# Optimization experiments

Measured on AMD Instinct MI355X. Metric: run time of the kernel, lower is better.

Reference implementation:

```python
import jax, jax.numpy as jnp
import numpy as np

# Model dims: nSet=48, nItemMax=80, input feat=512,
# D = baseChn*max_channel_ratio = 128 = head_size, H = num_heads = 2.
S, N, DIN = 48, 80, 512
D = 128
H, HS = 2, 128
EPS = 1e-3  # layer_normalization epsilon (non-set-norm branch)

def _w(key, fi, fo):
    return jax.random.normal(key, (fi, fo), jnp.float32) / np.sqrt(fi)

def setup_inputs() -> dict:
    key = jax.random.key(0)
    ks = jax.random.split(key, 20)
    sizes = jax.random.randint(ks[0], (S,), 1, N + 1)
    x = jax.random.normal(ks[1], (S, N, DIN), jnp.float32)
    item_mask = (jnp.arange(N)[None, :] < sizes[:, None]).astype(jnp.float32)
    x = x * item_mask[:, :, None]  # zero-pad invalid items (drives ==0 masks)
    return {
        "x": x,
        "x_size": sizes.astype(jnp.float32),
        # trainable MLP (fc1/fc2/fc3, gelu, no bias)
        "W1": _w(ks[2], DIN, 512),
        "W2": _w(ks[3], 512, 256),
        "W3": _w(ks[4], 256, D),
        # encoder self-attention layer
        "Wq_s": _w(ks[5], D, H * HS),
        "Wk_s": _w(ks[6], D, H * HS),
        "Wv_s": _w(ks[7], D, H * HS),
        "Wh_s": _w(ks[8], H * HS, HS),
        "Wfc_e": _w(ks[9], D, D),
        # decoder cross-set attention layer
        "Wq_c": _w(ks[10], D, H * HS),
        "Wk_c": _w(ks[11], D, H * HS),
        "Wv_c": _w(ks[12], D, H * HS),
        "Wh_c": _w(ks[13], H * HS, HS),
        "Wfc_d": _w(ks[14], D, D),
        # cross_set_score
        "Wcs": _w(ks[15], D, H * HS),
        "Wcs2": _w(ks[16], H, 1),
    }

def _gelu(z):
    return jax.nn.gelu(z, approximate=False)  # tf.nn.gelu default

def _item_norm(x):
    # layer_normalization with is_set_norm=False: per-item LN, zero padded rows
    mean = jnp.mean(x, axis=-1, keepdims=True)
    std = jnp.std(x, axis=-1, keepdims=True)
    norm = (x - mean) / (std + EPS)
    keep = jnp.sum(x, axis=-1, keepdims=True) != 0
    return jnp.where(keep, norm, jnp.zeros_like(x))

def _masked_softmax(s):
    # faithful to source: mask entries where raw score == 0
    m = s != 0
    e = jnp.where(m, jnp.exp(s - jnp.max(s, axis=-1, keepdims=True)), 0.0)
    return e / (jnp.sum(e, axis=-1, keepdims=True) + 1e-10)

def _mha(q_in, kv_in, Wq, Wk, Wv, Wh):
    # q_in/kv_in: [S, S, N, D]
    q = (q_in @ Wq).reshape(S, S, N, H, HS)
    k = (kv_in @ Wk).reshape(S, S, N, H, HS)
    v = (kv_in @ Wv).reshape(S, S, N, H, HS)
    s = jnp.einsum('xynhd,xymhd->xyhnm', q, k) / np.sqrt(HS)
    a = _masked_softmax(s)
    o = jnp.einsum('xyhnm,xymhd->xynhd', a, v).reshape(S, S, N, H * HS)
    return o @ Wh  # -> [S, S, N, HS]

def reference(x, x_size, W1, W2, W3, Wq_s, Wk_s, Wv_s, Wh_s, Wfc_e,
              Wq_c, Wk_c, Wv_c, Wh_c, Wfc_d, Wcs, Wcs2):
    # item-wise MLP projection: feat -> 512 -> 256 -> 128
    h = _gelu(_gelu(_gelu(x @ W1) @ W2) @ W3)  # [S, N, D]
    # pairwise set grid [nSet_x, nSet_y, nItemMax, D]
    x4 = jnp.broadcast_to(h[:, None], (S, S, N, D))
    # encoder: self-attention over items within each (i,j) pair
    z = _item_norm(x4)
    x4 = x4 + _mha(z, z, Wq_s, Wk_s, Wv_s, Wh_s)
    z = _item_norm(x4)
    x4 = x4 + _gelu(z @ Wfc_e)
    # decoder: cross-set attention, out[i,j] = Attn(q=z[i,j], kv=z[j,i])
    z = _item_norm(x4)
    x4 = x4 + _mha(z, jnp.transpose(z, (1, 0, 2, 3)), Wq_c, Wk_c, Wv_c, Wh_c)
    z = _item_norm(x4)
    x4 = x4 + _gelu(z @ Wfc_d)
    # cross_set_score: pairwise ReLU-matmul, set-size normalized
    xh = (x4 @ Wcs).reshape(S, S, N, H, HS).transpose(0, 1, 3, 2, 4)  # [j,i,h,n,d]
    A = jax.nn.relu(jnp.einsum('jihnd,ijhmd->jihnm', xh, xh) / np.sqrt(HS))
    sc = A.sum((-1, -2)) / x_size[None, :, None] / x_size[:, None, None]  # [S,S,H]
    return sc @ Wcs2  # [S, S, 1]
```

## Files before the change

### kernel.cpp

```cpp
#include <hip/hip_runtime.h>
#include <hip/hip_bf16.h>


#define SS 48
#define NI 80

typedef unsigned short us;
typedef __attribute__((ext_vector_type(8))) short s8v;
typedef __attribute__((ext_vector_type(4))) float f4v;

#define MFMA(a,b,c) __builtin_amdgcn_mfma_f32_16x16x32_bf16((a),(b),(c),0,0,0)

__device__ __forceinline__ float gelu_f(float x){
  return 0.5f * x * (1.0f + erff(x * 0.7071067811865475f));
}
__device__ __forceinline__ us f2b(float f){
  __hip_bfloat16 b = __float2bfloat16(f);
  return reinterpret_cast<us&>(b);
}
__device__ __forceinline__ s8v zero8(){ s8v v = {0,0,0,0,0,0,0,0}; return v; }
__device__ __forceinline__ void gl16(const void* g, void* l){
  __builtin_amdgcn_global_load_lds(
      (const __attribute__((address_space(1))) void*)g,
      (__attribute__((address_space(3))) void*)l, 16, 0, 0);
}

template<int ABF16, int OUTF32>
__global__ __launch_bounds__(256) void mgemm_k(const void* __restrict__ Ap,
    const float* __restrict__ B, void* __restrict__ Cp, int N, int K)
{
  __shared__ __align__(16) char lds[10240];
  char* As = lds; char* Bs = lds + 5120;
  const int t = threadIdx.x;
  const int wv = t >> 6, lm = t & 15, lh = (t >> 4) & 3;
  const int bx = blockIdx.x, by = blockIdx.y;
  const int ar = wv*16 + lm, r0 = wv*16 + lh*4;
  f4v acc[4];
#pragma unroll
  for (int ct = 0; ct < 4; ++ct) acc[ct] = {0.f,0.f,0.f,0.f};
  const int rA = t >> 2, kcA = (t & 3) << 3;
  const int kkB = t >> 3, nnB = (t & 7) << 3;
  for (int k0 = 0; k0 < K; k0 += 32) {
    __syncthreads();
    if (ABF16) {
      s8v v = *(const s8v*)((const us*)Ap + (size_t)(by*64 + rA)*K + k0 + kcA);
      *(s8v*)(As + rA*80 + kcA*2) = v;
    } else {
      const float* ap = (const float*)Ap + (size_t)(by*64 + rA)*K + k0 + kcA;
      float4 v0 = *(const float4*)ap, v1 = *(const float4*)(ap + 4);
      us tmp[8] = {f2b(v0.x),f2b(v0.y),f2b(v0.z),f2b(v0.w),
                   f2b(v1.x),f2b(v1.y),f2b(v1.z),f2b(v1.w)};
      *(s8v*)(As + rA*80 + kcA*2) = *(const s8v*)tmp;
    }
    {
      const float* bp = B + (size_t)(k0 + kkB)*N + bx*64 + nnB;
      float4 w0 = *(const float4*)bp, w1 = *(const float4*)(bp + 4);
      float w8[8] = {w0.x,w0.y,w0.z,w0.w,w1.x,w1.y,w1.z,w1.w};
#pragma unroll
      for (int q = 0; q < 8; ++q)
        *(us*)(Bs + (nnB + q)*80 + kkB*2) = f2b(w8[q]);
    }
    __syncthreads();
    s8v af = *(const s8v*)(As + ar*80 + lh*16);
#pragma unroll
    for (int ct = 0; ct < 4; ++ct) {
      s8v bf = *(const s8v*)(Bs + (ct*16 + lm)*80 + lh*16);
      acc[ct] = MFMA(af, bf, acc[ct]);
    }
  }
#pragma unroll
  for (int ct = 0; ct < 4; ++ct)
#pragma unroll
    for (int reg = 0; reg < 4; ++reg) {
      size_t r = by*64 + r0 + reg;
      int c = bx*64 + ct*16 + lm;
      float v = gelu_f(acc[ct][reg]);
      if (OUTF32) ((float*)Cp)[r*N + c] = v;
      else ((us*)Cp)[r*N + c] = f2b(v);
    }
}

__global__ __launch_bounds__(256) void qkv_k(const us* __restrict__ A,
    const float* __restrict__ Wq, const float* __restrict__ Wk,
    const float* __restrict__ Wv, us* __restrict__ Qb, us* __restrict__ Kb,
    us* __restrict__ VT)
{
  __shared__ __align__(16) char lds[10240];
  char* As = lds; char* Bs = lds + 5120;
  const int t = threadIdx.x;
  const int wv = t >> 6, lm = t & 15, lh = (t >> 4) & 3;
  const int bx = blockIdx.x, by = blockIdx.y;
  const int sel = bx >> 2, bxx = bx & 3;
  const float* B = sel == 0 ? Wq : (sel == 1 ? Wk : Wv);
  const int ar = wv*16 + lm, r0 = wv*16 + lh*4;
  f4v acc[4];
#pragma unroll
  for (int ct = 0; ct < 4; ++ct) acc[ct] = {0.f,0.f,0.f,0.f};
  const int rA = t >> 2, kcA = (t & 3) << 3;
  const int kkB = t >> 3, nnB = (t & 7) << 3;
#pragma unroll
  for (int k0 = 0; k0 < 128; k0 += 32) {
    __syncthreads();
    {
      s8v v = *(const s8v*)(A + (size_t)(by*64 + rA)*128 + k0 + kcA);
      *(s8v*)(As + rA*80 + kcA*2) = v;
      const float* bp = B + (size_t)(k0 + kkB)*256 + bxx*64 + nnB;
      float4 w0 = *(const float4*)bp, w1 = *(const float4*)(bp + 4);
      float w8[8] = {w0.x,w0.y,w0.z,w0.w,w1.x,w1.y,w1.z,w1.w};
#pragma unroll
      for (int q = 0; q < 8; ++q)
        *(us*)(Bs + (nnB + q)*80 + kkB*2) = f2b(w8[q]);
    }
    __syncthreads();
    s8v af = *(const s8v*)(As + ar*80 + lh*16);
#pragma unroll
    for (int ct = 0; ct < 4; ++ct) {
      s8v bf = *(const s8v*)(Bs + (ct*16 + lm)*80 + lh*16);
      acc[ct] = MFMA(af, bf, acc[ct]);
    }
  }
  if (sel < 2) {
    us* O = sel ? Kb : Qb;
#pragma unroll
    for (int ct = 0; ct < 4; ++ct)
#pragma unroll
      for (int reg = 0; reg < 4; ++reg)
        O[(size_t)(by*64 + r0 + reg)*256 + bxx*64 + ct*16 + lm] = f2b(acc[ct][reg]);
  } else {
#pragma unroll
    for (int ct = 0; ct < 4; ++ct)
#pragma unroll
      for (int reg = 0; reg < 4; ++reg) {
        int r = by*64 + r0 + reg;
        int s = r / 80, m = r % 80;
        int d = bxx*64 + ct*16 + lm;
        VT[((size_t)s*256 + d)*80 + m] = f2b(acc[ct][reg]);
      }
  }
}

__global__ __launch_bounds__(64) void norm_k(const float* __restrict__ in,
                                             us* __restrict__ out)
{
  const int r = blockIdx.x, t = threadIdx.x;
  float v0 = in[(size_t)r*128 + t];
  float v1 = in[(size_t)r*128 + t + 64];
  float sm = v0 + v1;
#pragma unroll
  for (int off = 1; off < 64; off <<= 1) sm += __shfl_xor(sm, off, 64);
  float mean = sm * (1.0f/128.0f);
  float d0 = v0 - mean, d1 = v1 - mean;
  float vs = d0*d0 + d1*d1;
#pragma unroll
  for (int off = 1; off < 64; off <<= 1) vs += __shfl_xor(vs, off, 64);
  float inv = 1.0f / (sqrtf(vs * (1.0f/128.0f)) + 1e-3f);
  bool keep = (sm != 0.0f);
  out[(size_t)r*128 + t]      = f2b(keep ? d0*inv : 0.0f);
  out[(size_t)r*128 + t + 64] = f2b(keep ? d1*inv : 0.0f);
}

__global__ __launch_bounds__(128) void prep_k(
    const float* __restrict__ Wh_s, const float* __restrict__ Wfc_e,
    const float* __restrict__ Wh_c, const float* __restrict__ Wfc_d,
    const float* __restrict__ Wcs,  const float* __restrict__ Wv_s,
    const float* __restrict__ Wv_c,
    us* __restrict__ WfcTe, us* __restrict__ WfcTd,
    float* __restrict__ Wvh_s, float* __restrict__ Wvh_c,
    us* __restrict__ Mb)
{
  const int x = blockIdx.x, task = blockIdx.y, tid = threadIdx.x;
  if (task == 0) {
    WfcTe[x*128 + tid] = f2b(Wfc_e[(size_t)tid*128 + x]);
  } else if (task == 1) {
    WfcTd[x*128 + tid] = f2b(Wfc_d[(size_t)tid*128 + x]);
  } else if (task < 6) {
    int h = (task - 2) & 1;
    const float* Wv = task < 4 ? Wv_s : Wv_c;
    const float* Wh = task < 4 ? Wh_s : Wh_c;
    float* Wvh = task < 4 ? Wvh_s : Wvh_c;
    float acc = 0.f;
#pragma unroll 8
    for (int d = 0; d < 128; ++d)
      acc = fmaf(Wv[(size_t)x*256 + h*128 + d], Wh[(size_t)(h*128 + d)*128 + tid], acc);
    Wvh[(size_t)x*256 + h*128 + tid] = acc;
  } else {
    int h = task - 6;
    float acc = 0.f;
#pragma unroll 8
    for (int k = 0; k < 128; ++k)
      acc = fmaf(Wcs[(size_t)x*256 + h*128 + k], Wcs[(size_t)tid*256 + h*128 + k], acc);
    Mb[(size_t)h*16384 + x*128 + tid] = f2b(acc);
  }
}

__device__ __forceinline__ void attn4e(int a, int t,
    const us* __restrict__ Qg, const us* __restrict__ Kg,
    const us* __restrict__ VTg, const float* __restrict__ baseg,
    const us* __restrict__ WfcT,
    char* __restrict__ X, char* __restrict__ Y, f4v x4[8])
{
  const int wv = t >> 6, lane = t & 63, lm = t & 15, lh = (t >> 4) & 3;
  const int ar = wv*16 + lm, r0 = wv*16 + lh*4;
  const float isq = 0.08838834764831845f;
  const int b = a;
#pragma unroll
  for (int dt = 0; dt < 8; ++dt) x4[dt] = (f4v){0.f,0.f,0.f,0.f};

#pragma unroll 1
  for (int h = 0; h < 2; ++h) {
    if (h == 1) __syncthreads();
#pragma unroll
    for (int c = 0; c < 4; ++c) {
      int chunk = wv*4 + c;
      int row = chunk*4 + (lane >> 4);
      int scb = ((lane & 15) << 4) ^ ((row & 7) << 4);
      gl16(Kg + (((size_t)(b*NI + row)) << 8) + h*128 + (scb >> 1), X + chunk*1024);
    }
    s8v qf[4];
    {
      const us* qrow = Qg + (((size_t)(a*NI + ar)) << 8) + h*128 + lh*8;
#pragma unroll
      for (int ks = 0; ks < 4; ++ks) qf[ks] = *(const s8v*)(qrow + ks*32);
    }
    __syncthreads();
    f4v sA[5];
#pragma unroll
    for (int nt = 0; nt < 5; ++nt) {
      int row = nt*16 + lm;
      f4v acc = (f4v){0.f,0.f,0.f,0.f};
#pragma unroll
      for (int ks = 0; ks < 4; ++ks) {
        s8v kf = *(const s8v*)(X + row*256 + ((ks*64 + lh*16) ^ ((row & 7) << 4)));
        acc = MFMA(qf[ks], kf, acc);
      }
      sA[nt] = acc;
    }
#pragma unroll
    for (int reg = 0; reg < 4; ++reg) {
      int r = r0 + reg;
      float sv[5];
#pragma unroll
      for (int nt = 0; nt < 5; ++nt) sv[nt] = sA[nt][reg] * isq;
      float mx = sv[0];
#pragma unroll
      for (int nt = 1; nt < 5; ++nt) mx = fmaxf(mx, sv[nt]);
#pragma unroll
      for (int off = 1; off < 16; off <<= 1) mx = fmaxf(mx, __shfl_xor(mx, off, 64));
      float e[5], sum = 0.f;
#pragma unroll
      for (int nt = 0; nt < 5; ++nt) {
        e[nt] = (sv[nt] != 0.f) ? __expf(sv[nt] - mx) : 0.f;
        sum += e[nt];
      }
#pragma unroll
      for (int off = 1; off < 16; off <<= 1) sum += __shfl_xor(sum, off, 64);
      float inv = 1.f / (sum + 1e-10f);
#pragma unroll
      for (int nt = 0; nt < 5; ++nt)
        *(us*)(Y + r*256 + ((2*(nt*16 + lm)) ^ ((r & 7) << 4))) = f2b(e[nt] * inv);
    }
    s8v pf0 = *(const s8v*)(Y + ar*256 + ((lh*16) ^ ((ar & 7) << 4)));
    s8v pf1 = *(const s8v*)(Y + ar*256 + ((64 + lh*16) ^ ((ar & 7) << 4)));
    s8v pf2 = zero8();
    if (lh < 2)
      pf2 = *(const s8v*)(Y + ar*256 + ((128 + lh*16) ^ ((ar & 7) << 4)));
    __syncthreads();
#pragma unroll
    for (int c = 0; c < 4; ++c) {
      int chunk = wv*4 + c;
      int L = chunk*1024 + lane*16;
      int rv = L / 160;
      int rem = L - rv*160;
      int cv = (rem >> 4) - (rv % 10); if (cv < 0) cv += 10;
      gl16(VTg + ((size_t)(b*256 + h*128 + rv))*80 + (cv << 3), X + chunk*1024);
    }
    __syncthreads();
#pragma unroll
    for (int dt = 0; dt < 8; ++dt) {
      int row = dt*16 + lm;
      int rm = (row % 10) << 4;
      int o0 = lh*16 + rm; if (o0 >= 160) o0 -= 160;
      x4[dt] = MFMA(pf0, *(const s8v*)(X + row*160 + o0), x4[dt]);
      int o1 = 64 + lh*16 + rm; if (o1 >= 160) o1 -= 160;
      x4[dt] = MFMA(pf1, *(const s8v*)(X + row*160 + o1), x4[dt]);
      s8v v2 = zero8();
      if (lh < 2) {
        int o2 = 128 + lh*16 + rm; if (o2 >= 160) o2 -= 160;
        v2 = *(const s8v*)(X + row*160 + o2);
      }
      x4[dt] = MFMA(pf2, v2, x4[dt]);
    }
    if (h == 1) {
#pragma unroll
      for (int reg = 0; reg < 4; ++reg) {
        int r = r0 + reg;
#pragma unroll
        for (int dt = 0; dt < 8; ++dt)
          x4[dt][reg] += baseg[(((size_t)(a*NI + r)) << 7) + dt*16 + lm];
      }
    }
  }

  __syncthreads();
  for (int chunk = wv; chunk < 16; chunk += 5) {
    int row = chunk*4 + (lane >> 4);
    int scb = ((lane & 15) << 4) ^ ((row & 7) << 4);
    gl16(WfcT + (size_t)row*128 + (scb >> 1), X + chunk*1024);
  }
#pragma unroll
  for (int reg = 0; reg < 4; ++reg) {
    int r = r0 + reg;
    float sm = 0.f;
#pragma unroll
    for (int dt = 0; dt < 8; ++dt) sm += x4[dt][reg];
#pragma unroll
    for (int off = 1; off < 16; off <<= 1) sm += __shfl_xor(sm, off, 64);
    float mean = sm * (1.0f/128.0f);
    float vs = 0.f;
#pragma unroll
    for (int dt = 0; dt < 8; ++dt) { float d = x4[dt][reg] - mean; vs = fmaf(d, d, vs); }
#pragma unroll
    for (int off = 1; off < 16; off <<= 1) vs += __shfl_xor(vs, off, 64);
    float inv = 1.f / (sqrtf(vs * (1.0f/128.0f)) + 1e-3f);
    bool keep = (sm != 0.f);
#pragma unroll
    for (int dt = 0; dt < 8; ++dt)
      *(us*)(Y + r*256 + ((2*(dt*16 + lm)) ^ ((r & 7) << 4))) = f2b(keep ? (x4[dt][reg]-mean)*inv : 0.f);
  }
  s8v zf[4];
#pragma unroll
  for (int ks = 0; ks < 4; ++ks)
    zf[ks] = *(const s8v*)(Y + ar*256 + ((ks*64 + lh*16) ^ ((ar & 7) << 4)));
  __syncthreads();
#pragma unroll
  for (int dt = 0; dt < 4; ++dt) {
    int row = dt*16 + lm;
    f4v acc = (f4v){0.f,0.f,0.f,0.f};
#pragma unroll
    for (int ks = 0; ks < 4; ++ks) {
      s8v wfr = *(const s8v*)(X + row*256 + ((ks*64 + lh*16) ^ ((row & 7) << 4)));
      acc = MFMA(zf[ks], wfr, acc);
    }
#pragma unroll
    for (int reg = 0; reg < 4; ++reg) x4[dt][reg] += gelu_f(acc[reg]);
  }
  __syncthreads();
  for (int chunk = wv; chunk < 16; chunk += 5) {
    int row = chunk*4 + (lane >> 4);
    int scb = ((lane & 15) << 4) ^ ((row & 7) << 4);
    gl16(WfcT + (size_t)(row + 64)*128 + (scb >> 1), X + chunk*1024);
  }
  __syncthreads();
#pragma unroll
  for (int dt = 4; dt < 8; ++dt) {
    int row = dt*16 + lm;
    int r2 = row - 64;
    f4v acc = (f4v){0.f,0.f,0.f,0.f};
#pragma unroll
    for (int ks = 0; ks < 4; ++ks) {
      s8v wfr = *(const s8v*)(X + r2*256 + ((ks*64 + lh*16) ^ ((row & 7) << 4)));
      acc = MFMA(zf[ks], wfr, acc);
    }
#pragma unroll
    for (int reg = 0; reg < 4; ++reg) x4[dt][reg] += gelu_f(acc[reg]);
  }
}

__global__ __launch_bounds__(320) void enc_k(
    const us* __restrict__ Qg, const us* __restrict__ Kg,
    const us* __restrict__ VTg, const float* __restrict__ hb,
    const us* __restrict__ WfcT, float* __restrict__ e2p,
    us* __restrict__ z3b)
{
  __shared__ __align__(16) char X[20480];
  __shared__ __align__(16) char Y[20480];
  const int t = threadIdx.x;
  const int wv = t >> 6, lm = t & 15, lh = (t >> 4) & 3;
  const int r0 = wv*16 + lh*4;
  const int i = blockIdx.x;
  f4v x4[8];
  attn4e(i, t, Qg, Kg, VTg, hb, WfcT, X, Y, x4);
#pragma unroll
  for (int reg = 0; reg < 4; ++reg) {
    int r = r0 + reg;
    size_t gb = ((size_t)(i*NI + r)) << 7;
    float tmp[8]; float sm = 0.f;
#pragma unroll
    for (int dt = 0; dt < 8; ++dt) { tmp[dt] = x4[dt][reg]; sm += tmp[dt]; }
    *(float4*)(e2p + gb + lm*8)     = make_float4(tmp[0],tmp[1],tmp[2],tmp[3]);
    *(float4*)(e2p + gb + lm*8 + 4) = make_float4(tmp[4],tmp[5],tmp[6],tmp[7]);
#pragma unroll
    for (int off = 1; off < 16; off <<= 1) sm += __shfl_xor(sm, off, 64);
    float mean = sm * (1.0f/128.0f);
    float vs = 0.f;
#pragma unroll
    for (int dt = 0; dt < 8; ++dt) { float d = tmp[dt] - mean; vs = fmaf(d, d, vs); }
#pragma unroll
    for (int off = 1; off < 16; off <<= 1) vs += __shfl_xor(vs, off, 64);
    float inv = 1.f / (sqrtf(vs * (1.0f/128.0f)) + 1e-3f);
    bool keep = (sm != 0.f);
#pragma unroll
    for (int dt = 0; dt < 8; ++dt)
      z3b[gb + dt*16 + lm] = f2b(keep ? (tmp[dt]-mean)*inv : 0.f);
  }
}

__global__ __launch_bounds__(640, 2) void dec8_k(
    const us* __restrict__ Qg, const us* __restrict__ Kg,
    const us* __restrict__ VTg, const float* __restrict__ e2p,
    const us* __restrict__ WfcT, us* __restrict__ x4g)
{
  __shared__ __align__(16) char L[155648];
  const int t = threadIdx.x;
  const int g = (t >= 320) ? 1 : 0;
  const int tg = t - g*320;
  const int wv = tg >> 6, wb = t >> 6;
  const int lane = t & 63, lm = t & 15, lh = (t >> 4) & 3;
  const int ar = wv*16 + lm, r0 = wv*16 + lh*4;
  const float isq = 0.08838834764831845f;
  const int a = blockIdx.x, b = blockIdx.y*2 + g;
  char* W  = L;
  char* S0 = L + 32768 + g*61440;
  char* S1 = S0 + 20480;
  char* Y  = S0 + 40960;

#define STG_K(DST, H)                                                        \
  { _Pragma("unroll") for (int c_ = 0; c_ < 4; ++c_) {                       \
      int ch_ = wv*4 + c_;                                                   \
      int rw_ = ch_*4 + (lane >> 4);                                         \
      int sc_ = ((lane & 15) << 4) ^ ((rw_ & 7) << 4);                       \
      gl16(Kg + (((size_t)(b*NI + rw_)) << 8) + (H)*128 + (sc_ >> 1),        \
           (DST) + ch_*1024); } }
#define STG_VT(DST, H)                                                       \
  { _Pragma("unroll") for (int c_ = 0; c_ < 4; ++c_) {                       \
      int ch_ = wv*4 + c_;                                                   \
      int L_ = ch_*1024 + lane*16;                                           \
      int rv_ = L_ / 160;                                                    \
      int cv_ = ((L_ - rv_*160) >> 4) - (rv_ % 10); if (cv_ < 0) cv_ += 10;  \
      gl16(VTg + ((size_t)(b*256 + (H)*128 + rv_))*80 + (cv_ << 3),          \
           (DST) + ch_*1024); } }
#define QKSM(KS, H)                                                          \
  { s8v qf_[4];                                                              \
    { const us* qr_ = Qg + (((size_t)(a*NI + ar)) << 8) + (H)*128 + lh*8;    \
      _Pragma("unroll") for (int ks = 0; ks < 4; ++ks)                       \
        qf_[ks] = *(const s8v*)(qr_ + ks*32); }                              \
    f4v sA_[5];                                                              \
    _Pragma("unroll") for (int nt = 0; nt < 5; ++nt) {                       \
      int rw_ = nt*16 + lm;                                                  \
      f4v ac_ = (f4v){0.f,0.f,0.f,0.f};                                      \
      _Pragma("unroll") for (int ks = 0; ks < 4; ++ks) {                     \
        s8v kf_ = *(const s8v*)((KS) + rw_*256 +                             \
                                ((ks*64 + lh*16) ^ ((rw_ & 7) << 4)));       \
        ac_ = MFMA(qf_[ks], kf_, ac_); }                                     \
      sA_[nt] = ac_; }                                                       \
    _Pragma("unroll") for (int reg = 0; reg < 4; ++reg) {                    \
      int r_ = r0 + reg;                                                     \
      float sv_[5];                                                          \
      _Pragma("unroll") for (int nt = 0; nt < 5; ++nt)                       \
        sv_[nt] = sA_[nt][reg] * isq;                                        \
      float mx_ = sv_[0];                                                    \
      _Pragma("unroll") for (int nt = 1; nt < 5; ++nt)                       \
        mx_ = fmaxf(mx_, sv_[nt]);                                           \
      _Pragma("unroll") for (int of_ = 1; of_ < 16; of_ <<= 1)               \
        mx_ = fmaxf(mx_, __shfl_xor(mx_, of_, 64));                          \
      float e_[5], su_ = 0.f;                                                \
      _Pragma("unroll") for (int nt = 0; nt < 5; ++nt) {                     \
        e_[nt] = (sv_[nt] != 0.f) ? __expf(sv_[nt] - mx_) : 0.f;             \
        su_ += e_[nt]; }                                                     \
      _Pragma("unroll") for (int of_ = 1; of_ < 16; of_ <<= 1)               \
        su_ += __shfl_xor(su_, of_, 64);                                     \
      float iv_ = 1.f / (su_ + 1e-10f);                                      \
      _Pragma("unroll") for (int nt = 0; nt < 5; ++nt)                       \
        *(us*)(Y + r_*256 + ((2*(nt*16 + lm)) ^ ((r_ & 7) << 4))) =          \
            f2b(e_[nt] * iv_); } }
#define PV(VS)                                                               \
  { s8v pf0_ = *(const s8v*)(Y + ar*256 + ((lh*16) ^ ((ar & 7) << 4)));      \
    s8v pf1_ = *(const s8v*)(Y + ar*256 + ((64 + lh*16) ^ ((ar & 7) << 4))); \
    s8v pf2_ = zero8();                                                      \
    if (lh < 2)                                                              \
      pf2_ = *(const s8v*)(Y + ar*256 + ((128 + lh*16) ^ ((ar & 7) << 4)));  \
    _Pragma("unroll") for (int dt = 0; dt < 8; ++dt) {                       \
      int rw_ = dt*16 + lm;                                                  \
      int rm_ = (rw_ % 10) << 4;                                             \
      int o0_ = lh*16 + rm_; if (o0_ >= 160) o0_ -= 160;                     \
      x4[dt] = MFMA(pf0_, *(const s8v*)((VS) + rw_*160 + o0_), x4[dt]);      \
      int o1_ = 64 + lh*16 + rm_; if (o1_ >= 160) o1_ -= 160;                \
      x4[dt] = MFMA(pf1_, *(const s8v*)((VS) + rw_*160 + o1_), x4[dt]);      \
      s8v v2_ = zero8();                                                     \
      if (lh < 2) { int o2_ = 128 + lh*16 + rm_;                             \
        if (o2_ >= 160) o2_ -= 160;                                          \
        v2_ = *(const s8v*)((VS) + rw_*160 + o2_); }                         \
      x4[dt] = MFMA(pf2_, v2_, x4[dt]); } }

  f4v x4[8];
#pragma unroll
  for (int dt = 0; dt < 8; ++dt) x4[dt] = (f4v){0.f,0.f,0.f,0.f};

  for (int ch = wb; ch < 32; ch += 10) {
    int row = ch*4 + (lane >> 4);
    int scb = ((lane & 15) << 4) ^ ((row & 7) << 4);
    gl16(WfcT + (size_t)row*128 + (scb >> 1), W + ch*1024);
  }
  STG_K(S0, 0);
  __syncthreads();
  STG_VT(S1, 0);
  QKSM(S0, 0);
  __syncthreads();
  STG_K(S0, 1);
  PV(S1);
  __syncthreads();
  STG_VT(S1, 1);
  QKSM(S0, 1);
  __syncthreads();
  PV(S1);
#pragma unroll
  for (int reg = 0; reg < 4; ++reg) {
    const f4v* bp = (const f4v*)(e2p + (((size_t)(a*NI + r0 + reg)) << 7) + lm*8);
    f4v bb0 = bp[0], bb1 = bp[1];
#pragma unroll
    for (int dt = 0; dt < 4; ++dt) {
      x4[dt][reg]   += bb0[dt];
      x4[dt+4][reg] += bb1[dt];
    }
  }
#pragma unroll
  for (int reg = 0; reg < 4; ++reg) {
    int r = r0 + reg;
    float sm = 0.f;
#pragma unroll
    for (int dt = 0; dt < 8; ++dt) sm += x4[dt][reg];
#pragma unroll
    for (int off = 1; off < 16; off <<= 1) sm += __shfl_xor(sm, off, 64);
    float mean = sm * (1.0f/128.0f);
    float vs = 0.f;
#pragma unroll
    for (int dt = 0; dt < 8; ++dt) { float d = x4[dt][reg] - mean; vs = fmaf(d, d, vs); }
#pragma unroll
    for (int off = 1; off < 16; off <<= 1) vs += __shfl_xor(vs, off, 64);
    float inv = 1.f / (sqrtf(vs * (1.0f/128.0f)) + 1e-3f);
    bool keep = (sm != 0.f);
#pragma unroll
    for (int dt = 0; dt < 8; ++dt)
      *(us*)(Y + r*256 + ((2*(dt*16 + lm)) ^ ((r & 7) << 4))) = f2b(keep ? (x4[dt][reg]-mean)*inv : 0.f);
  }
  {
    s8v zf[4];
#pragma unroll
    for (int ks = 0; ks < 4; ++ks)
      zf[ks] = *(const s8v*)(Y + ar*256 + ((ks*64 + lh*16) ^ ((ar & 7) << 4)));
#pragma unroll
    for (int dt = 0; dt < 8; ++dt) {
      int row = dt*16 + lm;
      f4v ac = (f4v){0.f,0.f,0.f,0.f};
#pragma unroll
      for (int ks = 0; ks < 4; ++ks) {
        s8v wf = *(const s8v*)(W + row*256 + ((ks*64 + lh*16) ^ ((row & 7) << 4)));
        ac = MFMA(zf[ks], wf, ac);
      }
#pragma unroll
      for (int reg = 0; reg < 4; ++reg) x4[dt][reg] += gelu_f(ac[reg]);
    }
  }
#pragma unroll
  for (int reg = 0; reg < 4; ++reg) {
    int r = r0 + reg;
#pragma unroll
    for (int dt = 0; dt < 8; ++dt)
      *(us*)(Y + r*256 + ((2*(dt*16 + lm)) ^ ((r & 7) << 4))) = f2b(x4[dt][reg]);
  }
  {
    char* dst = (char*)(x4g + ((size_t)a*SS + b)*10240);
#pragma unroll
    for (int q = 0; q < 4; ++q) {
      int c = lane + q*64;
      int row = wv*16 + (c >> 4);
      int cb = (c & 15) << 4;
      s8v v = *(const s8v*)(Y + row*256 + (cb ^ ((row & 7) << 4)));
      *(s8v*)(dst + row*256 + cb) = v;
    }
  }
#undef STG_K
#undef STG_VT
#undef QKSM
#undef PV
}

__global__ __launch_bounds__(640, 2) void ugemm3_k(const us* __restrict__ x4g,
    const us* __restrict__ Mb, us* __restrict__ Ugc)
{
  __shared__ __align__(16) char As[2][20480];
  __shared__ __align__(16) char Bs[2][16384];
  const int t = threadIdx.x;
  const int g = (t >= 320) ? 1 : 0;
  const int tg = t - g*320;
  const int wv = tg >> 6, lm = t & 15, lh = (t >> 4) & 3;
  const int ar = wv*16 + lm, r0 = wv*16 + lh*4;
  int bid = blockIdx.x*2 + g;
  int ii = (int)(0.5f*(97.0f - sqrtf(9409.0f - 8.0f*(float)bid)));
  if (ii > 47) ii = 47; if (ii < 0) ii = 0;
  while (ii*SS - ii*(ii-1)/2 > bid) --ii;
  while ((ii+1)*SS - (ii+1)*ii/2 <= bid) ++ii;
  const int i = ii, j = ii + (bid - (ii*SS - ii*(ii-1)/2));
  const us* A = x4g + ((size_t)j*SS + i)*10240;

#pragma unroll
  for (int c = 0; c < 4; ++c) {
    int chunk = wv*4 + c;
    int row = chunk*4 + ((t & 63) >> 4);
    int scb = ((t & 15) << 4) ^ ((row & 7) << 4);
    gl16(A + (size_t)row*128 + (scb >> 1), As[g] + chunk*1024);
  }
  f4v acc[16];
#pragma unroll
  for (int ct = 0; ct < 16; ++ct) acc[ct] = (f4v){0.f,0.f,0.f,0.f};
#pragma unroll 1
  for (int k0 = 0; k0 < 128; k0 += 32) {
    if (k0) __syncthreads();
    for (int c = wv; c < 16; c += 5) {
      int row = c*16 + ((t & 63) >> 2);
      int colb = (t & 3) << 4;
      int scb = colb ^ ((row & 3) << 4);
      gl16(Mb + (size_t)row*128 + k0 + (scb >> 1), Bs[g] + c*1024);
    }
    __syncthreads();
    int ks = k0 >> 5;
    s8v af = *(const s8v*)(As[g] + ar*256 + ((ks*64 + lh*16) ^ ((ar & 7) << 4)));
#pragma unroll
    for (int ct = 0; ct < 16; ++ct) {
      int row = ct*16 + lm;
      s8v bf = *(const s8v*)(Bs[g] + row*64 + ((lh*16) ^ ((row & 3) << 4)));
      acc[ct] = MFMA(af, bf, acc[ct]);
    }
  }
#pragma unroll
  for (int ct = 0; ct < 16; ++ct)
#pragma unroll
    for (int reg = 0; reg < 4; ++reg)
      Ugc[((size_t)bid*80 + r0 + reg)*256 + ct*16 + lm] = f2b(acc[ct][reg]);
}

__global__ __launch_bounds__(640, 2) void p4_k(
    const us* __restrict__ x4g, const us* __restrict__ Ugc,
    const float* __restrict__ Wcs2, const float* __restrict__ xsg,
    float* __restrict__ outg)
{
  __shared__ __align__(16) char Xi[2][20480];
  __shared__ __align__(16) char Xu[2][40960];
  __shared__ float red[2][10];
  const int t = threadIdx.x;
  const int g = (t >= 320) ? 1 : 0;
  const int tg = t - g*320;
  const int wv = tg >> 6, lm = t & 15, lh = (t >> 4) & 3;
  const int ar = wv*16 + lm, r0 = wv*16 + lh*4;
  const float isq = 0.08838834764831845f;

  int bid0 = blockIdx.x*2 + g;
  int bid = (bid0 & 7) * 147 + (bid0 >> 3);
  int ii = (int)(0.5f*(97.0f - sqrtf(9409.0f - 8.0f*(float)bid)));
  if (ii > 47) ii = 47; if (ii < 0) ii = 0;
  while (ii*SS - ii*(ii-1)/2 > bid) --ii;
  while ((ii+1)*SS - (ii+1)*ii/2 <= bid) ++ii;
  const int i = ii, j = ii + (bid - (ii*SS - ii*(ii-1)/2));
  const size_t xpid = (size_t)i*SS + j;

#pragma unroll
  for (int c = 0; c < 4; ++c) {
    int chunk = wv*4 + c;
    int row = chunk*4 + ((t & 63) >> 4);
    int scb = ((t & 15) << 4) ^ ((row & 7) << 4);
    gl16(x4g + xpid*10240 + (size_t)row*128 + (scb >> 1), Xi[g] + chunk*1024);
    gl16(Ugc + ((size_t)bid*80 + row)*256 + (scb >> 1), Xu[g] + chunk*1024);
    gl16(Ugc + ((size_t)bid*80 + row)*256 + 128 + (scb >> 1),
         Xu[g] + 20480 + chunk*1024);
  }
  __syncthreads();
  s8v xf[4];
#pragma unroll
  for (int ks = 0; ks < 4; ++ks)
    xf[ks] = *(const s8v*)(Xi[g] + ar*256 + ((ks*64 + lh*16) ^ ((ar & 7) << 4)));

  float sc[2];
#pragma unroll 1
  for (int h = 0; h < 2; ++h) {
    const char* Xh = Xu[g] + h*20480;
    float loc = 0.f;
#pragma unroll
    for (int nt = 0; nt < 5; ++nt) {
      int brow = nt*16 + lm;
      f4v acc = (f4v){0.f,0.f,0.f,0.f};
#pragma unroll
      for (int ks = 0; ks < 4; ++ks) {
        s8v bf = *(const s8v*)(Xh + brow*256 + ((ks*64 + lh*16) ^ ((brow & 7) << 4)));
        acc = MFMA(xf[ks], bf, acc);
      }
#pragma unroll
      for (int reg = 0; reg < 4; ++reg) loc += fmaxf(acc[reg]*isq, 0.f);
    }
    sc[h] = loc;
  }
#pragma unroll
  for (int off = 1; off < 64; off <<= 1) {
    sc[0] += __shfl_xor(sc[0], off, 64);
    sc[1] += __shfl_xor(sc[1], off, 64);
  }
  if ((tg & 63) == 0) { red[g][wv] = sc[0]; red[g][wv + 5] = sc[1]; }
  __syncthreads();
  if (tg == 0) {
    float s0 = red[g][0]+red[g][1]+red[g][2]+red[g][3]+red[g][4];
    float s1 = red[g][5]+red[g][6]+red[g][7]+red[g][8]+red[g][9];
    float val = (s0*Wcs2[0] + s1*Wcs2[1]) / (xsg[i]*xsg[j]);
    outg[i*SS + j] = val;
    outg[j*SS + i] = val;
  }
}

extern "C" void kernel_launch(void* const* d_in, const int* in_sizes, int n_in,
                              void* d_out, int out_size, void* d_ws, size_t ws_size,
                              hipStream_t stream)
{
  (void)in_sizes; (void)n_in; (void)out_size; (void)ws_size;
  const float* x     = (const float*)d_in[0];
  const float* xs    = (const float*)d_in[1];
  const float* W1    = (const float*)d_in[2];
  const float* W2    = (const float*)d_in[3];
  const float* W3    = (const float*)d_in[4];
  const float* Wq_s  = (const float*)d_in[5];
  const float* Wk_s  = (const float*)d_in[6];
  const float* Wv_s  = (const float*)d_in[7];
  const float* Wh_s  = (const float*)d_in[8];
  const float* Wfc_e = (const float*)d_in[9];
  const float* Wq_c  = (const float*)d_in[10];
  const float* Wk_c  = (const float*)d_in[11];
  const float* Wv_c  = (const float*)d_in[12];
  const float* Wh_c  = (const float*)d_in[13];
  const float* Wfc_d = (const float*)d_in[14];
  const float* Wcs   = (const float*)d_in[15];
  const float* Wcs2  = (const float*)d_in[16];
  float* out = (float*)d_out;

  char* w = (char*)d_ws;
  us* h1b     = (us*)w;    w += (size_t)3840*512*2;
  us* h2b     = (us*)w;    w += (size_t)3840*256*2;
  float* hb   = (float*)w; w += (size_t)3840*128*4;
  us* zb16    = (us*)w;    w += (size_t)3840*128*2;
  us* z3b     = (us*)w;    w += (size_t)3840*128*2;
  float* e2p  = (float*)w; w += (size_t)3840*128*4;
  us* Qb      = (us*)w;    w += (size_t)3840*256*2;
  us* Kb      = (us*)w;    w += (size_t)3840*256*2;
  us* VT      = (us*)w;    w += (size_t)48*256*80*2;
  us* WfcTe   = (us*)w;    w += 16384*2;
  us* WfcTd   = (us*)w;    w += 16384*2;
  us* Mb      = (us*)w;    w += 32768*2;
  float* Wvh_s = (float*)w; w += 32768*4;
  float* Wvh_c = (float*)w; w += 32768*4;
  us* x4g     = (us*)w;    w += (size_t)2304*10240*2;
  us* Ugc     = (us*)w;    w += (size_t)1176*80*256*2;

  hipLaunchKernelGGL(prep_k, dim3(128, 8), dim3(128), 0, stream,
                     Wh_s, Wfc_e, Wh_c, Wfc_d, Wcs, Wv_s, Wv_c,
                     WfcTe, WfcTd, Wvh_s, Wvh_c, Mb);
  hipLaunchKernelGGL((mgemm_k<0,0>), dim3(8,60), dim3(256), 0, stream,
                     (const void*)x, W1, (void*)h1b, 512, 512);
  hipLaunchKernelGGL((mgemm_k<1,0>), dim3(4,60), dim3(256), 0, stream,
                     (const void*)h1b, W2, (void*)h2b, 256, 512);
  hipLaunchKernelGGL((mgemm_k<1,1>), dim3(2,60), dim3(256), 0, stream,
                     (const void*)h2b, W3, (void*)hb, 128, 256);
  hipLaunchKernelGGL(norm_k, dim3(3840), dim3(64), 0, stream, hb, zb16);
  hipLaunchKernelGGL(qkv_k, dim3(12,60), dim3(256), 0, stream,
                     zb16, Wq_s, Wk_s, Wvh_s, Qb, Kb, VT);
  hipLaunchKernelGGL(enc_k, dim3(48), dim3(320), 0, stream,
                     Qb, Kb, VT, hb, WfcTe, e2p, z3b);
  hipLaunchKernelGGL(qkv_k, dim3(12,60), dim3(256), 0, stream,
                     z3b, Wq_c, Wk_c, Wvh_c, Qb, Kb, VT);
  hipLaunchKernelGGL(dec8_k, dim3(48,24), dim3(640), 0, stream,
                     Qb, Kb, VT, e2p, WfcTd, x4g);
  hipLaunchKernelGGL(ugemm3_k, dim3(588), dim3(640), 0, stream, x4g, Mb, Ugc);
  hipLaunchKernelGGL(p4_k, dim3(588), dim3(640), 0, stream,
                     x4g, Ugc, Wcs2, xs, out);
}
```

Before: 251.4 us.

## Fuse U-projection GEMM into pairwise score kernel via shared memory

New measurement: 239.9 us (median of 3 runs). -4.6%, faster.

```diff
diff --git a/kernel.cpp b/kernel.cpp
--- a/kernel.cpp
+++ b/kernel.cpp
@@ -585,116 +585,92 @@
 #undef PV
 }
 
-__global__ __launch_bounds__(640, 2) void ugemm3_k(const us* __restrict__ x4g,
-    const us* __restrict__ Mb, us* __restrict__ Ugc)
-{
-  __shared__ __align__(16) char As[2][20480];
-  __shared__ __align__(16) char Bs[2][16384];
-  const int t = threadIdx.x;
-  const int g = (t >= 320) ? 1 : 0;
-  const int tg = t - g*320;
-  const int wv = tg >> 6, lm = t & 15, lh = (t >> 4) & 3;
-  const int ar = wv*16 + lm, r0 = wv*16 + lh*4;
-  int bid = blockIdx.x*2 + g;
-  int ii = (int)(0.5f*(97.0f - sqrtf(9409.0f - 8.0f*(float)bid)));
-  if (ii > 47) ii = 47; if (ii < 0) ii = 0;
-  while (ii*SS - ii*(ii-1)/2 > bid) --ii;
-  while ((ii+1)*SS - (ii+1)*ii/2 <= bid) ++ii;
-  const int i = ii, j = ii + (bid - (ii*SS - ii*(ii-1)/2));
-  const us* A = x4g + ((size_t)j*SS + i)*10240;
-
-#pragma unroll
-  for (int c = 0; c < 4; ++c) {
-    int chunk = wv*4 + c;
-    int row = chunk*4 + ((t & 63) >> 4);
-    int scb = ((t & 15) << 4) ^ ((row & 7) << 4);
-    gl16(A + (size_t)row*128 + (scb >> 1), As[g] + chunk*1024);
-  }
-  f4v acc[16];
-#pragma unroll
-  for (int ct = 0; ct < 16; ++ct) acc[ct] = (f4v){0.f,0.f,0.f,0.f};
-#pragma unroll 1
-  for (int k0 = 0; k0 < 128; k0 += 32) {
-    if (k0) __syncthreads();
-    for (int c = wv; c < 16; c += 5) {
-      int row = c*16 + ((t & 63) >> 2);
-      int colb = (t & 3) << 4;
-      int scb = colb ^ ((row & 3) << 4);
-      gl16(Mb + (size_t)row*128 + k0 + (scb >> 1), Bs[g] + c*1024);
-    }
-    __syncthreads();
-    int ks = k0 >> 5;
-    s8v af = *(const s8v*)(As[g] + ar*256 + ((ks*64 + lh*16) ^ ((ar & 7) << 4)));
-#pragma unroll
-    for (int ct = 0; ct < 16; ++ct) {
-      int row = ct*16 + lm;
-      s8v bf = *(const s8v*)(Bs[g] + row*64 + ((lh*16) ^ ((row & 3) << 4)));
-      acc[ct] = MFMA(af, bf, acc[ct]);
-    }
-  }
-#pragma unroll
-  for (int ct = 0; ct < 16; ++ct)
-#pragma unroll
-    for (int reg = 0; reg < 4; ++reg)
-      Ugc[((size_t)bid*80 + r0 + reg)*256 + ct*16 + lm] = f2b(acc[ct][reg]);
-}
-
-__global__ __launch_bounds__(640, 2) void p4_k(
-    const us* __restrict__ x4g, const us* __restrict__ Ugc,
+__global__ __launch_bounds__(320) void up_k(
+    const us* __restrict__ x4g, const us* __restrict__ Mb,
     const float* __restrict__ Wcs2, const float* __restrict__ xsg,
     float* __restrict__ outg)
 {
-  __shared__ __align__(16) char Xi[2][20480];
-  __shared__ __align__(16) char Xu[2][40960];
-  __shared__ float red[2][10];
+  __shared__ __align__(16) char As[20480];
+  __shared__ __align__(16) char Bs[16384];
+  __shared__ __align__(16) char Xi[20480];
+  __shared__ __align__(16) char Xu[40960];
+  __shared__ float red[10];
   const int t = threadIdx.x;
-  const int g = (t >= 320) ? 1 : 0;
-  const int tg = t - g*320;
-  const int wv = tg >> 6, lm = t & 15, lh = (t >> 4) & 3;
+  const int wv = t >> 6, lane = t & 63, lm = t & 15, lh = (t >> 4) & 3;
   const int ar = wv*16 + lm, r0 = wv*16 + lh*4;
   const float isq = 0.08838834764831845f;
 
-  int bid0 = blockIdx.x*2 + g;
+  int bid0 = blockIdx.x;
   int bid = (bid0 & 7) * 147 + (bid0 >> 3);
   int ii = (int)(0.5f*(97.0f - sqrtf(9409.0f - 8.0f*(float)bid)));
   if (ii > 47) ii = 47; if (ii < 0) ii = 0;
   while (ii*SS - ii*(ii-1)/2 > bid) --ii;
   while ((ii+1)*SS - (ii+1)*ii/2 <= bid) ++ii;
   const int i = ii, j = ii + (bid - (ii*SS - ii*(ii-1)/2));
-  const size_t xpid = (size_t)i*SS + j;
+  const us* Aji = x4g + ((size_t)j*SS + i)*10240;
+  const us* Aij = x4g + ((size_t)i*SS + j)*10240;
 
 #pragma unroll
   for (int c = 0; c < 4; ++c) {
     int chunk = wv*4 + c;
-    int row = chunk*4 + ((t & 63) >> 4);
-    int scb = ((t & 15) << 4) ^ ((row & 7) << 4);
-    gl16(x4g + xpid*10240 + (size_t)row*128 + (scb >> 1), Xi[g] + chunk*1024);
-    gl16(Ugc + ((size_t)bid*80 + row)*256 + (scb >> 1), Xu[g] + chunk*1024);
-    gl16(Ugc + ((size_t)bid*80 + row)*256 + 128 + (scb >> 1),
-         Xu[g] + 20480 + chunk*1024);
+    int row = chunk*4 + (lane >> 4);
+    int scb = ((lane & 15) << 4) ^ ((row & 7) << 4);
+    gl16(Aji + (size_t)row*128 + (scb >> 1), As + chunk*1024);
+    gl16(Aij + (size_t)row*128 + (scb >> 1), Xi + chunk*1024);
+  }
+  f4v acc[16];
+#pragma unroll
+  for (int ct = 0; ct < 16; ++ct) acc[ct] = (f4v){0.f,0.f,0.f,0.f};
+#pragma unroll 1
+  for (int k0 = 0; k0 < 128; k0 += 32) {
+    if (k0) __syncthreads();
+    for (int c = wv; c < 16; c += 5) {
+      int row = c*16 + (lane >> 2);
+      int colb = (lane & 3) << 4;
+      int scb = colb ^ ((row & 3) << 4);
+      gl16(Mb + (size_t)row*128 + k0 + (scb >> 1), Bs + c*1024);
+    }
+    __syncthreads();
+    int ks = k0 >> 5;
+    s8v af = *(const s8v*)(As + ar*256 + ((ks*64 + lh*16) ^ ((ar & 7) << 4)));
+#pragma unroll
+    for (int ct = 0; ct < 16; ++ct) {
+      int row = ct*16 + lm;
+      s8v bf = *(const s8v*)(Bs + row*64 + ((lh*16) ^ ((row & 3) << 4)));
+      acc[ct] = MFMA(af, bf, acc[ct]);
+    }
+  }
+#pragma unroll
+  for (int ct = 0; ct < 16; ++ct) {
+    int h = ct >> 3;
+    int cl = (ct & 7)*16 + lm;
+#pragma unroll
+    for (int reg = 0; reg < 4; ++reg) {
+      int row = r0 + reg;
+      *(us*)(Xu + h*20480 + row*256 + ((2*cl) ^ ((row & 7) << 4))) = f2b(acc[ct][reg]);
+    }
   }
   __syncthreads();
   s8v xf[4];
 #pragma unroll
   for (int ks = 0; ks < 4; ++ks)
-    xf[ks] = *(const s8v*)(Xi[g] + ar*256 + ((ks*64 + lh*16) ^ ((ar & 7) << 4)));
-
+    xf[ks] = *(const s8v*)(Xi + ar*256 + ((ks*64 + lh*16) ^ ((ar & 7) << 4)));
   float sc[2];
 #pragma unroll 1
   for (int h = 0; h < 2; ++h) {
-    const char* Xh = Xu[g] + h*20480;
+    const char* Xh = Xu + h*20480;
     float loc = 0.f;
 #pragma unroll
     for (int nt = 0; nt < 5; ++nt) {
       int brow = nt*16 + lm;
-      f4v acc = (f4v){0.f,0.f,0.f,0.f};
+      f4v ac = (f4v){0.f,0.f,0.f,0.f};
 #pragma unroll
       for (int ks = 0; ks < 4; ++ks) {
         s8v bf = *(const s8v*)(Xh + brow*256 + ((ks*64 + lh*16) ^ ((brow & 7) << 4)));
-        acc = MFMA(xf[ks], bf, acc);
+        ac = MFMA(xf[ks], bf, ac);
       }
 #pragma unroll
-      for (int reg = 0; reg < 4; ++reg) loc += fmaxf(acc[reg]*isq, 0.f);
+      for (int reg = 0; reg < 4; ++reg) loc += fmaxf(ac[reg]*isq, 0.f);
     }
     sc[h] = loc;
   }
@@ -703,11 +679,11 @@
     sc[0] += __shfl_xor(sc[0], off, 64);
     sc[1] += __shfl_xor(sc[1], off, 64);
   }
-  if ((tg & 63) == 0) { red[g][wv] = sc[0]; red[g][wv + 5] = sc[1]; }
-  __syncthreads();
-  if (tg == 0) {
-    float s0 = red[g][0]+red[g][1]+red[g][2]+red[g][3]+red[g][4];
-    float s1 = red[g][5]+red[g][6]+red[g][7]+red[g][8]+red[g][9];
+  if ((t & 63) == 0) { red[wv] = sc[0]; red[wv + 5] = sc[1]; }
+  __syncthreads();
+  if (t == 0) {
+    float s0 = red[0]+red[1]+red[2]+red[3]+red[4];
+    float s1 = red[5]+red[6]+red[7]+red[8]+red[9];
     float val = (s0*Wcs2[0] + s1*Wcs2[1]) / (xsg[i]*xsg[j]);
     outg[i*SS + j] = val;
     outg[j*SS + i] = val;
@@ -754,7 +730,6 @@
   float* Wvh_s = (float*)w; w += 32768*4;
   float* Wvh_c = (float*)w; w += 32768*4;
   us* x4g     = (us*)w;    w += (size_t)2304*10240*2;
-  us* Ugc     = (us*)w;    w += (size_t)1176*80*256*2;
 
   hipLaunchKernelGGL(prep_k, dim3(128, 8), dim3(128), 0, stream,
                      Wh_s, Wfc_e, Wh_c, Wfc_d, Wcs, Wv_s, Wv_c,
@@ -774,7 +749,6 @@
                      z3b, Wq_c, Wk_c, Wvh_c, Qb, Kb, VT);
   hipLaunchKernelGGL(dec8_k, dim3(48,24), dim3(640), 0, stream,
                      Qb, Kb, VT, e2p, WfcTd, x4g);
-  hipLaunchKernelGGL(ugemm3_k, dim3(588), dim3(640), 0, stream, x4g, Mb, Ugc);
-  hipLaunchKernelGGL(p4_k, dim3(588), dim3(640), 0, stream,
-                     x4g, Ugc, Wcs2, xs, out);
-}
+  hipLaunchKernelGGL(up_k, dim3(1176), dim3(320), 0, stream,
+                     x4g, Mb, Wcs2, xs, out);
+}
```
